# Optimization experiments

Hardware: AMD Instinct MI355X
Metric: run time of the kernel (lower is better)

## Reference

```python
import jax, jax.numpy as jnp
import numpy as np

IN_NC = 32
OUT_NC = 32
EXPAND = 2
HID = IN_NC * EXPAND          # 64
K = 3                         # depthwise kernel
EPS = 1e-5
R1 = IN_NC * HID              # end of pointwise-1 weights
R2 = R1 + HID * K * K         # end of depthwise weights
R3 = R2 + HID * OUT_NC        # total hyper params = 4672


def _bn(t, g, b):
    # BatchNorm2d in training mode over the flattened (b*fh*fw) batch:
    # stats over all axes except the channel axis (axis=3 of [b,fh,fw,C,H,W]).
    ax = (0, 1, 2, 4, 5)
    m = jnp.mean(t, axis=ax, keepdims=True)
    v = jnp.mean((t - m) ** 2, axis=ax, keepdims=True)
    sh = (1, 1, 1, -1, 1, 1)
    return (t - m) * jax.lax.rsqrt(v + EPS) * g.reshape(sh) + b.reshape(sh)


def _relu6(t):
    return jnp.clip(t, 0.0, 6.0)


def setup_inputs() -> dict:
    key = jax.random.key(0)
    k0, k1 = jax.random.split(key)
    x = jax.random.normal(k0, (8, IN_NC, 256, 256), dtype=jnp.float32)
    s = jax.random.normal(k1, (8, R3, 32, 32), dtype=jnp.float32) * 0.1
    return {
        'x': x,
        's': s,
        'gamma1': jnp.ones((HID,), jnp.float32),
        'beta1': jnp.zeros((HID,), jnp.float32),
        'gamma2': jnp.ones((HID,), jnp.float32),
        'beta2': jnp.zeros((HID,), jnp.float32),
        'gamma3': jnp.ones((OUT_NC,), jnp.float32),
        'beta3': jnp.zeros((OUT_NC,), jnp.float32),
    }


def reference(x, s, gamma1, beta1, gamma2, beta2, gamma3, beta3):
    b, c, h, w = x.shape
    fh, fw = s.shape[-2], s.shape[-1]
    ph, pw = h // fh, w // fw          # patch size
    kh, kw = ph + 2, pw + 2            # patch + reflect halo of 1

    # reflect-pad then extract overlapping [kh,kw] patches on a [ph,pw] grid
    xp = jnp.pad(x, ((0, 0), (0, 0), (1, 1), (1, 1)), mode='reflect')
    ri = (jnp.arange(fh) * ph)[:, None] + jnp.arange(kh)   # [fh,kh]
    ci = (jnp.arange(fw) * pw)[:, None] + jnp.arange(kw)   # [fw,kw]
    patches = xp[:, :, ri][:, :, :, :, ci]                 # [b,c,fh,kh,fw,kw]
    patches = patches.transpose(0, 2, 4, 1, 3, 5)          # [b,fh,fw,c,kh,kw]

    sw = s.transpose(0, 2, 3, 1)                           # [b,fh,fw,R3]

    # stage 1: per-patch 1x1 expand conv (in_nc -> hidden)
    w1 = sw[..., :R1].reshape(b, fh, fw, HID, c)
    y = jnp.einsum('bfgoc,bfgchw->bfgohw', w1, patches)    # [b,fh,fw,HID,kh,kw]
    y = _relu6(_bn(y, gamma1, beta1))

    # stage 2: per-patch depthwise 3x3 conv (valid), stride 1 -> [ph,pw]
    w2 = sw[..., R1:R2].reshape(b, fh, fw, HID, K, K)
    z = jnp.zeros((b, fh, fw, HID, ph, pw), y.dtype)
    for u in range(K):
        for v in range(K):
            z = z + w2[..., u, v, None, None] * y[..., u:u + ph, v:v + pw]
    z = _relu6(_bn(z, gamma2, beta2))

    # stage 3: per-patch 1x1 project conv (hidden -> out_nc)
    w3 = sw[..., R2:R3].reshape(b, fh, fw, OUT_NC, HID)
    o = jnp.einsum('bfgoc,bfgcpq->bfgopq', w3, z)          # [b,fh,fw,OUT_NC,ph,pw]
    o = _bn(o, gamma3, beta3)

    # reassemble patches: [b,fh,fw,C,ph,pw] -> [b,C,h,w]
    o = o.transpose(0, 3, 1, 4, 2, 5).reshape(b, OUT_NC, h, w)
    return x + o  # use_res_connect: stride==1 and in_nc==out_nc
```

## Files before the change

### kernel.cpp

```cpp
#include <hip/hip_runtime.h>

#define NT 256

constexpr int R1c = 2048;
constexpr int R2c = 2624;
constexpr float EPSc = 1e-5f;

constexpr int SLOTS1  = 0;
constexpr int SLOTS1Q = 4096;
constexpr int SLOTS2  = 8192;
constexpr int SLOTS2Q = 12288;
constexpr int SLOTS3  = 16384;
constexpr int SLOTS3Q = 18432;
constexpr int FIN1    = 20480;
constexpr int FIN2    = 20608;
constexpr int FIN3    = 20736;
constexpr int STATS_ZERO_FLOATS = 20480;

constexpr size_t ST2_OFF   = 131072;
constexpr size_t ST2_BYTES = 8ull * 1024 * 4672 * 2;
constexpr size_t ZB_OFF    = ST2_OFF + ST2_BYTES;
constexpr size_t ZB_BYTES  = 8192ull * 4096 * 2;
constexpr size_t OI_OFF    = ZB_OFF + ZB_BYTES;

__device__ __forceinline__ ushort f_to_bf16(float f) {
    union { float f; unsigned int i; } v; v.f = f;
    unsigned int r = (v.i + 0x7fffu + ((v.i >> 16) & 1u)) >> 16;
    return (ushort)r;
}
__device__ __forceinline__ float bf16_to_f(ushort u) {
    union { unsigned int i; float f; } v; v.i = ((unsigned int)u) << 16; return v.f;
}
__device__ __forceinline__ float bf16lo_to_f(unsigned int u) {
    union { unsigned int i; float f; } v; v.i = u << 16; return v.f;
}
__device__ __forceinline__ float bf16hi_to_f(unsigned int u) {
    union { unsigned int i; float f; } v; v.i = u & 0xffff0000u; return v.f;
}
__device__ __forceinline__ unsigned int pack_bf16(float lo, float hi) {
    return (unsigned int)f_to_bf16(lo) | ((unsigned int)f_to_bf16(hi) << 16);
}

typedef short bf16x8 __attribute__((ext_vector_type(8)));
typedef float f32x4  __attribute__((ext_vector_type(4)));
union FR { uint4 u4; bf16x8 v; ushort s[8]; };

__device__ __forceinline__ f32x4 mfma16(bf16x8 a, bf16x8 b, f32x4 c) {
    return __builtin_amdgcn_mfma_f32_16x16x32_bf16(a, b, c, 0, 0, 0);
}

__global__ __launch_bounds__(256)
void transpose_s_bf16p(const float* __restrict__ s, ushort* __restrict__ st) {
    __shared__ float tile[64][33];
    const int bi = blockIdx.z;
    const int p0 = blockIdx.x * 64;
    const int q0 = blockIdx.y * 32;
    const int tx = threadIdx.x, ty = threadIdx.y;
    const float* sb = s + (size_t)bi * 4672 * 1024;
    #pragma unroll
    for (int r = ty; r < 64; r += 8)
        tile[r][tx] = sb[(size_t)(p0 + r) * 1024 + q0 + tx];
    __syncthreads();
    unsigned int* stu = (unsigned int*)(st + (size_t)bi * 1024 * 4672);
    #pragma unroll
    for (int rr = ty; rr < 32; rr += 8) {
        int q = q0 + rr;
        unsigned int v = pack_bf16(tile[2*tx][rr], tile[2*tx + 1][rr]);
        stu[((size_t)q * 4672 + p0) / 2 + tx] = v;
    }
}


__global__ __launch_bounds__(NT, 4)
void k1_mf(const float* __restrict__ x, const ushort* __restrict__ st2,
           float* __restrict__ ws) {
    __shared__ ushort frB[4 * 3584];
    __shared__ float st1[128];
    const int t = threadIdx.x, blk = blockIdx.x;
    const int bi = blk >> 8, f = (blk >> 3) & 31, jb = blk & 7;
    const int g0 = jb * 4, slot = blk & 63;
    const int w = t >> 6, l = t & 63, l15 = l & 15, grp = l >> 4;

    if (t < 128) st1[t] = 0.f;
    {
        int p = t >> 6, e = t & 63;
        if ((e & 15) >= 4)
            ((uint4*)frB)[p * 448 + 384 + e] = make_uint4(0u, 0u, 0u, 0u);
    }
    const ushort* wp = st2 + (size_t)(bi * 1024 + f * 32 + g0 + w) * 4672;
    FR aw[4];
    #pragma unroll
    for (int m = 0; m < 4; m++) aw[m].u4 = ((const uint4*)wp)[(m * 16 + l15) * 4 + grp];

    const float* xb = x + (size_t)bi * 32 * 65536;
    for (int i = t; i < 3200; i += NT) {
        int c = i / 100, rem = i - c * 100;
        int r = rem / 10, seg = rem - r * 10;
        int row = f * 8 - 1 + r; row = row < 0 ? -row : (row > 255 ? 510 - row : row);
        int col0 = g0 * 8 - 4 + seg * 4;
        float v4[4];
        if (col0 >= 0 && col0 <= 252) {
            float4 vv = *(const float4*)(xb + (size_t)c * 65536 + row * 256 + col0);
            v4[0] = vv.x; v4[1] = vv.y; v4[2] = vv.z; v4[3] = vv.w;
        } else {
            #pragma unroll
            for (int d = 0; d < 4; d++) {
                int cc = col0 + d; cc = cc < 0 ? -cc : (cc > 255 ? 510 - cc : cc);
                v4[d] = xb[(size_t)c * 65536 + row * 256 + cc];
            }
        }
        int grpc = c >> 3, j = c & 7;
        #pragma unroll
        for (int d = 0; d < 4; d++) {
            int u = col0 + d - g0 * 8;
            ushort hv = f_to_bf16(v4[d]);
            #pragma unroll
            for (int p = 0; p < 4; p++) {
                int pc = u - 8 * p + 1;
                if (pc >= 0 && pc <= 9) {
                    int px = r * 10 + pc;
                    frB[p * 3584 + ((px >> 4) * 64 + grpc * 16 + (px & 15)) * 8 + j] = hv;
                }
            }
        }
    }
    __syncthreads();

    FR b[7];
    const uint4* bp = (const uint4*)(frB + w * 3584);
    #pragma unroll
    for (int n = 0; n < 7; n++) b[n].u4 = bp[n * 64 + l];
    float s4[16], q4[16];
    #pragma unroll
    for (int i = 0; i < 16; i++) { s4[i] = 0.f; q4[i] = 0.f; }
    #pragma unroll
    for (int m = 0; m < 4; m++) {
        #pragma unroll
        for (int n = 0; n < 7; n++) {
            f32x4 z = {0.f, 0.f, 0.f, 0.f};
            f32x4 c = mfma16(aw[m].v, b[n].v, z);
            #pragma unroll
            for (int r = 0; r < 4; r++) { float v = c[r]; s4[m*4+r] += v; q4[m*4+r] += v * v; }
        }
    }
    #pragma unroll
    for (int i = 0; i < 16; i++) {
        float sm = s4[i], qq = q4[i];
        #pragma unroll
        for (int msk = 1; msk <= 8; msk <<= 1) { sm += __shfl_xor(sm, msk); qq += __shfl_xor(qq, msk); }
        if (l15 == 0) {
            int ch = (i >> 2) * 16 + grp * 4 + (i & 3);
            atomicAdd(&st1[ch], sm);
            atomicAdd(&st1[64 + ch], qq);
        }
    }
    __syncthreads();
    if (t < 64) {
        atomicAdd(&ws[SLOTS1  + t * 64 + slot], st1[t]);
        atomicAdd(&ws[SLOTS1Q + t * 64 + slot], st1[64 + t]);
    }
}

__global__ __launch_bounds__(NT, 3)
void k2_mf(const float* __restrict__ x, const ushort* __restrict__ st2,
           ushort* __restrict__ zbuf, float* __restrict__ ws) {
    __shared__ ushort frB[4 * 3584];
    __shared__ unsigned int w2L[4 * 288];
    __shared__ float fin_s[128];
    const int t = threadIdx.x, blk = blockIdx.x;
    const int bi = blk >> 8, f = (blk >> 3) & 31, jb = blk & 7;
    const int g0 = jb * 4, slot = blk & 63;
    const int w = t >> 6, l = t & 63, l15 = l & 15, grp = l >> 4;
    const int patch = bi * 1024 + f * 32 + g0 + w;

    if (t < 128) fin_s[t] = ws[FIN1 + t];
    {
        int p = t >> 6, e = t & 63;
        if ((e & 15) >= 4)
            ((uint4*)frB)[p * 448 + 384 + e] = make_uint4(0u, 0u, 0u, 0u);
    }
    const ushort* wp = st2 + (size_t)patch * 4672;
    FR aw[4];
    #pragma unroll
    for (int m = 0; m < 4; m++) aw[m].u4 = ((const uint4*)wp)[(m * 16 + l15) * 4 + grp];
    for (int k = l; k < 288; k += 64) w2L[w * 288 + k] = ((const unsigned int*)(wp + R1c))[k];

    const float* xb = x + (size_t)bi * 32 * 65536;
    for (int i = t; i < 3200; i += NT) {
        int c = i / 100, rem = i - c * 100;
        int r = rem / 10, seg = rem - r * 10;
        int row = f * 8 - 1 + r; row = row < 0 ? -row : (row > 255 ? 510 - row : row);
        int col0 = g0 * 8 - 4 + seg * 4;
        float v4[4];
        if (col0 >= 0 && col0 <= 252) {
            float4 vv = *(const float4*)(xb + (size_t)c * 65536 + row * 256 + col0);
            v4[0] = vv.x; v4[1] = vv.y; v4[2] = vv.z; v4[3] = vv.w;
        } else {
            #pragma unroll
            for (int d = 0; d < 4; d++) {
                int cc = col0 + d; cc = cc < 0 ? -cc : (cc > 255 ? 510 - cc : cc);
                v4[d] = xb[(size_t)c * 65536 + row * 256 + cc];
            }
        }
        int grpc = c >> 3, j = c & 7;
        #pragma unroll
        for (int d = 0; d < 4; d++) {
            int u = col0 + d - g0 * 8;
            ushort hv = f_to_bf16(v4[d]);
            #pragma unroll
            for (int p = 0; p < 4; p++) {
                int pc = u - 8 * p + 1;
                if (pc >= 0 && pc <= 9) {
                    int px = r * 10 + pc;
                    frB[p * 3584 + ((px >> 4) * 64 + grpc * 16 + (px & 15)) * 8 + j] = hv;
                }
            }
        }
    }
    __syncthreads();

    FR b[7];
    const uint4* bp = (const uint4*)(frB + w * 3584);
    #pragma unroll
    for (int n = 0; n < 7; n++) b[n].u4 = bp[n * 64 + l];

    ushort* slice = frB + w * 3584;
    const ushort* w2u = (const ushort*)(w2L + w * 288);
    const int ch_l = l >> 2, quad = l & 3, p0 = quad * 2;
    float zsum[4], zsq[4];
    ushort* zp0 = zbuf + (size_t)patch * 4096;

    #pragma unroll
    for (int m = 0; m < 4; m++) {
        #pragma unroll
        for (int n = 0; n < 7; n++) {
            f32x4 z = {0.f, 0.f, 0.f, 0.f};
            f32x4 c = mfma16(aw[m].v, b[n].v, z);
            int px = n * 16 + l15;
            if (px < 100) {
                #pragma unroll
                for (int r = 0; r < 4; r++) {
                    int ch = m * 16 + grp * 4 + r;
                    float v = fminf(fmaxf(c[r] * fin_s[ch] + fin_s[64 + ch], 0.f), 6.f);
                    slice[(grp * 4 + r) * 102 + px] = f_to_bf16(v);
                }
            }
        }
        float yv[4][10];
        const unsigned int* sl32 = (const unsigned int*)slice;
        #pragma unroll
        for (int rr = 0; rr < 4; rr++) {
            int base = ch_l * 51 + (p0 + rr) * 5;
            #pragma unroll
            for (int k = 0; k < 5; k++) {
                unsigned int u = sl32[base + k];
                yv[rr][2*k] = bf16lo_to_f(u); yv[rr][2*k+1] = bf16hi_to_f(u);
            }
        }
        float wt[9];
        #pragma unroll
        for (int k = 0; k < 9; k++) wt[k] = bf16_to_f(w2u[(m * 16 + ch_l) * 9 + k]);
        float za[2][8];
        #pragma unroll
        for (int rr = 0; rr < 2; rr++)
            #pragma unroll
            for (int q = 0; q < 8; q++) za[rr][q] = 0.f;
        #pragma unroll
        for (int u = 0; u < 3; u++)
            #pragma unroll
            for (int v = 0; v < 3; v++) {
                float wv = wt[u * 3 + v];
                #pragma unroll
                for (int rr = 0; rr < 2; rr++)
                    #pragma unroll
                    for (int q = 0; q < 8; q++)
                        za[rr][q] += wv * yv[rr + u][q + v];
            }
        float zs = 0.f, zq = 0.f;
        #pragma unroll
        for (int rr = 0; rr < 2; rr++)
            #pragma unroll
            for (int q = 0; q < 8; q++) { float v = za[rr][q]; zs += v; zq += v * v; }
        zsum[m] = zs; zsq[m] = zq;
        ushort* zp = zp0 + (m * 16 + ch_l) * 64 + p0 * 8;
        uint4 pk0, pk1;
        pk0.x = pack_bf16(za[0][0], za[0][1]); pk0.y = pack_bf16(za[0][2], za[0][3]);
        pk0.z = pack_bf16(za[0][4], za[0][5]); pk0.w = pack_bf16(za[0][6], za[0][7]);
        pk1.x = pack_bf16(za[1][0], za[1][1]); pk1.y = pack_bf16(za[1][2], za[1][3]);
        pk1.z = pack_bf16(za[1][4], za[1][5]); pk1.w = pack_bf16(za[1][6], za[1][7]);
        *(uint4*)zp = pk0;
        *(uint4*)(zp + 8) = pk1;
    }
    __syncthreads();
    if (t < 128) fin_s[t] = 0.f;
    __syncthreads();
    #pragma unroll
    for (int m = 0; m < 4; m++) {
        float zs = zsum[m], zq = zsq[m];
        zs += __shfl_xor(zs, 1); zs += __shfl_xor(zs, 2);
        zq += __shfl_xor(zq, 1); zq += __shfl_xor(zq, 2);
        if (quad == 0) {
            atomicAdd(&fin_s[m * 16 + ch_l], zs);
            atomicAdd(&fin_s[64 + m * 16 + ch_l], zq);
        }
    }
    __syncthreads();
    if (t < 64) {
        atomicAdd(&ws[SLOTS2  + t * 64 + slot], fin_s[t]);
        atomicAdd(&ws[SLOTS2Q + t * 64 + slot], fin_s[64 + t]);
    }
}

__global__ __launch_bounds__(NT, 4)
void k3_mf(const ushort* __restrict__ zbuf, const ushort* __restrict__ st2,
           ushort* __restrict__ oi, float* __restrict__ ws) {
    __shared__ ushort zL[4 * 4224];
    __shared__ float fin2[128];
    __shared__ float st3[64];
    const int t = threadIdx.x, blk = blockIdx.x;
    const int bi = blk >> 8, f = (blk >> 3) & 31, jb = blk & 7;
    const int g0 = jb * 4, slot = blk & 63;
    const int w = t >> 6, l = t & 63, l15 = l & 15, grp = l >> 4;
    const int patch = bi * 1024 + f * 32 + g0 + w;

    if (t < 128) fin2[t] = ws[FIN2 + t];
    if (t >= 128 && t < 192) st3[t - 128] = 0.f;
    const ushort* wp = st2 + (size_t)patch * 4672;
    FR aw[2][2];
    #pragma unroll
    for (int m = 0; m < 2; m++)
        #pragma unroll
        for (int ks = 0; ks < 2; ks++)
            aw[m][ks].u4 = ((const uint4*)(wp + R2c))[(m * 16 + l15) * 8 + ks * 4 + grp];
    __syncthreads();

    const uint4* zsrc = (const uint4*)(zbuf + (size_t)patch * 4096);
    unsigned int* zd = (unsigned int*)zL;
    #pragma unroll
    for (int it = 0; it < 8; it++) {
        int i = l + 64 * it;
        uint4 v = zsrc[i];
        int ch = i >> 3, px0 = (i & 7) * 8;
        float a2 = fin2[ch], b2 = fin2[64 + ch];
        unsigned int uu[4] = {v.x, v.y, v.z, v.w};
        int base = w * 2112 + (ch * 66 + px0) / 2;
        #pragma unroll
        for (int k = 0; k < 4; k++) {
            float lo = fminf(fmaxf(bf16lo_to_f(uu[k]) * a2 + b2, 0.f), 6.f);
            float hi = fminf(fmaxf(bf16hi_to_f(uu[k]) * a2 + b2, 0.f), 6.f);
            zd[base + k] = pack_bf16(lo, hi);
        }
    }
    FR bfr[2][4];
    #pragma unroll
    for (int ks = 0; ks < 2; ks++)
        #pragma unroll
        for (int n = 0; n < 4; n++)
            #pragma unroll
            for (int j = 0; j < 8; j++)
                bfr[ks][n].s[j] = zL[w * 4224 + (ks * 32 + grp * 8 + j) * 66 + n * 16 + l15];

    float s4[2][4], q4[2][4];
    #pragma unroll
    for (int m = 0; m < 2; m++)
        #pragma unroll
        for (int r = 0; r < 4; r++) { s4[m][r] = 0.f; q4[m][r] = 0.f; }
    #pragma unroll
    for (int m = 0; m < 2; m++)
        #pragma unroll
        for (int n = 0; n < 4; n++) {
            f32x4 z = {0.f, 0.f, 0.f, 0.f};
            f32x4 c = mfma16(aw[m][0].v, bfr[0][n].v, z);
            c = mfma16(aw[m][1].v, bfr[1][n].v, c);
            #pragma unroll
            for (int r = 0; r < 4; r++) {
                float v = c[r];
                s4[m][r] += v; q4[m][r] += v * v;
                int oc = m * 16 + grp * 4 + r;
                int px = n * 16 + l15, p = px >> 3, q = px & 7;
                oi[((size_t)(bi * 32 + oc) * 256 + f * 8 + p) * 256 + (g0 + w) * 8 + q] = f_to_bf16(v);
            }
        }
    #pragma unroll
    for (int m = 0; m < 2; m++)
        #pragma unroll
        for (int r = 0; r < 4; r++) {
            float sm = s4[m][r], qq = q4[m][r];
            #pragma unroll
            for (int msk = 1; msk <= 8; msk <<= 1) { sm += __shfl_xor(sm, msk); qq += __shfl_xor(qq, msk); }
            if (l15 == 0) {
                int oc = m * 16 + grp * 4 + r;
                atomicAdd(&st3[oc], sm);
                atomicAdd(&st3[32 + oc], qq);
            }
        }
    __syncthreads();
    if (t < 32) {
        atomicAdd(&ws[SLOTS3  + t * 64 + slot], st3[t]);
        atomicAdd(&ws[SLOTS3Q + t * 64 + slot], st3[32 + t]);
    }
}

__global__ __launch_bounds__(NT, 8)
void k4_st(const float* __restrict__ x, const float* __restrict__ ws,
           const ushort* __restrict__ oi, float* __restrict__ out) {
    #pragma unroll
    for (int it = 0; it < 8; it++) {
        size_t e = ((size_t)(blockIdx.x * NT + threadIdx.x) + (size_t)it * (2048 * NT)) * 4;
        int oc = (int)((e >> 16) & 31);
        float a3 = ws[FIN3 + oc], b3 = ws[FIN3 + 32 + oc];
        uint2 ov = *(const uint2*)(oi + e);
        float4 xv = *(const float4*)(x + e);
        float4 r;
        r.x = xv.x + bf16lo_to_f(ov.x) * a3 + b3;
        r.y = xv.y + bf16hi_to_f(ov.x) * a3 + b3;
        r.z = xv.z + bf16lo_to_f(ov.y) * a3 + b3;
        r.w = xv.w + bf16hi_to_f(ov.y) * a3 + b3;
        *(float4*)(out + e) = r;
    }
}

__global__ void finalize_k(float* __restrict__ ws, int stage,
                           const float* __restrict__ gamma, const float* __restrict__ beta) {
    int ch = threadIdx.x;
    int nch = (stage == 3) ? 32 : 64;
    if (ch >= nch) return;
    int so = (stage == 1) ? SLOTS1  : (stage == 2) ? SLOTS2  : SLOTS3;
    int sq = (stage == 1) ? SLOTS1Q : (stage == 2) ? SLOTS2Q : SLOTS3Q;
    int fo = (stage == 1) ? FIN1    : (stage == 2) ? FIN2    : FIN3;
    float N = (stage == 1) ? 819200.0f : 524288.0f;
    float sm = 0.f, qq = 0.f;
    for (int j = 0; j < 64; j++) { sm += ws[so + ch*64 + j]; qq += ws[sq + ch*64 + j]; }
    float mean = sm / N;
    float var  = qq / N - mean * mean;
    float rstd = rsqrtf(var + EPSc);
    float a = rstd * gamma[ch];
    ws[fo + ch]       = a;
    ws[fo + nch + ch] = beta[ch] - mean * a;
}

extern "C" void kernel_launch(void* const* d_in, const int* in_sizes, int n_in,
                              void* d_out, int out_size, void* d_ws, size_t ws_size,
                              hipStream_t stream) {
    const float* x  = (const float*)d_in[0];
    const float* s  = (const float*)d_in[1];
    const float* g1 = (const float*)d_in[2];
    const float* b1 = (const float*)d_in[3];
    const float* g2 = (const float*)d_in[4];
    const float* b2 = (const float*)d_in[5];
    const float* g3 = (const float*)d_in[6];
    const float* b3 = (const float*)d_in[7];
    float* out = (float*)d_out;
    float* ws  = (float*)d_ws;

    hipMemsetAsync(d_ws, 0, STATS_ZERO_FLOATS * sizeof(float), stream);

    ushort* st2 = (ushort*)((char*)d_ws + ST2_OFF);
    ushort* zb  = (ushort*)((char*)d_ws + ZB_OFF);
    ushort* oi  = (ushort*)((char*)d_ws + OI_OFF);

    transpose_s_bf16p<<<dim3(73, 32, 8), dim3(32, 8), 0, stream>>>(s, st2);
    k1_mf<<<2048, NT, 0, stream>>>(x, st2, ws);
    finalize_k<<<1, 64, 0, stream>>>(ws, 1, g1, b1);
    k2_mf<<<2048, NT, 0, stream>>>(x, st2, zb, ws);
    finalize_k<<<1, 64, 0, stream>>>(ws, 2, g2, b2);
    k3_mf<<<2048, NT, 0, stream>>>(zb, st2, oi, ws);
    finalize_k<<<1, 64, 0, stream>>>(ws, 3, g3, b3);
    k4_st<<<2048, NT, 0, stream>>>(x, ws, oi, out);
}
```

Baseline: 298.8 us.

## Store stage-1 expand output in bf16 and skip recompute in stage 2

Stage 1 now writes its pointwise-expand result (pre-BN) as bf16 into a workspace buffer, staged through shared memory, and a new stage-2 kernel reads that buffer instead of reloading x and redoing the MFMA expand conv. This trades the recompute and the gather of x patches for roughly 109 MB of extra global writes and reads. The path is only taken when the workspace is large enough, with the old path kept as a fallback. The output buffer aliases the new y region, which is safe because y is consumed before stage 3 writes.

Result: faster. 284.8 us (-4.7%).

```diff
diff --git a/kernel.cpp b/kernel.cpp
--- a/kernel.cpp
+++ b/kernel.cpp
@@ -21,7 +21,10 @@
 constexpr size_t ST2_BYTES = 8ull * 1024 * 4672 * 2;
 constexpr size_t ZB_OFF    = ST2_OFF + ST2_BYTES;
 constexpr size_t ZB_BYTES  = 8192ull * 4096 * 2;
-constexpr size_t OI_OFF    = ZB_OFF + ZB_BYTES;
+constexpr size_t Y_OFF     = ZB_OFF + ZB_BYTES;
+constexpr size_t Y_BYTES   = 8192ull * 13312;
+constexpr size_t NEED_Y    = Y_OFF + Y_BYTES;
+constexpr size_t OI_OFF    = Y_OFF;
 
 __device__ __forceinline__ ushort f_to_bf16(float f) {
     union { float f; unsigned int i; } v; v.f = f;
@@ -70,16 +73,17 @@
     }
 }
 
-
+template<int SY>
 __global__ __launch_bounds__(NT, 4)
 void k1_mf(const float* __restrict__ x, const ushort* __restrict__ st2,
-           float* __restrict__ ws) {
+           ushort* __restrict__ ybuf, float* __restrict__ ws) {
     __shared__ ushort frB[4 * 3584];
     __shared__ float st1[128];
     const int t = threadIdx.x, blk = blockIdx.x;
     const int bi = blk >> 8, f = (blk >> 3) & 31, jb = blk & 7;
     const int g0 = jb * 4, slot = blk & 63;
     const int w = t >> 6, l = t & 63, l15 = l & 15, grp = l >> 4;
+    const int patch = bi * 1024 + f * 32 + g0 + w;
 
     if (t < 128) st1[t] = 0.f;
     {
@@ -87,7 +91,7 @@
         if ((e & 15) >= 4)
             ((uint4*)frB)[p * 448 + 384 + e] = make_uint4(0u, 0u, 0u, 0u);
     }
-    const ushort* wp = st2 + (size_t)(bi * 1024 + f * 32 + g0 + w) * 4672;
+    const ushort* wp = st2 + (size_t)patch * 4672;
     FR aw[4];
     #pragma unroll
     for (int m = 0; m < 4; m++) aw[m].u4 = ((const uint4*)wp)[(m * 16 + l15) * 4 + grp];
@@ -130,6 +134,11 @@
     const uint4* bp = (const uint4*)(frB + w * 3584);
     #pragma unroll
     for (int n = 0; n < 7; n++) b[n].u4 = bp[n * 64 + l];
+
+    ushort* slice = frB + w * 3584;
+    unsigned int* sliceU = (unsigned int*)slice;
+    uint4* yb4 = SY ? (((uint4*)ybuf) + (size_t)patch * 832) : nullptr;
+
     float s4[16], q4[16];
     #pragma unroll
     for (int i = 0; i < 16; i++) { s4[i] = 0.f; q4[i] = 0.f; }
@@ -139,8 +148,19 @@
         for (int n = 0; n < 7; n++) {
             f32x4 z = {0.f, 0.f, 0.f, 0.f};
             f32x4 c = mfma16(aw[m].v, b[n].v, z);
-            #pragma unroll
-            for (int r = 0; r < 4; r++) { float v = c[r]; s4[m*4+r] += v; q4[m*4+r] += v * v; }
+            int px = n * 16 + l15;
+            #pragma unroll
+            for (int r = 0; r < 4; r++) {
+                float v = c[r]; s4[m*4+r] += v; q4[m*4+r] += v * v;
+                if (SY && px < 100) slice[(grp * 4 + r) * 106 + px] = f_to_bf16(v);
+            }
+        }
+        if (SY) {
+            for (int i = l; i < 208; i += 64) {
+                int ch2 = i / 13, sub = i - ch2 * 13;
+                int ub = ch2 * 53 + sub * 4;
+                yb4[m * 208 + i] = make_uint4(sliceU[ub], sliceU[ub+1], sliceU[ub+2], sliceU[ub+3]);
+            }
         }
     }
     #pragma unroll
@@ -158,6 +178,111 @@
     if (t < 64) {
         atomicAdd(&ws[SLOTS1  + t * 64 + slot], st1[t]);
         atomicAdd(&ws[SLOTS1Q + t * 64 + slot], st1[64 + t]);
+    }
+}
+
+__global__ __launch_bounds__(NT, 4)
+void k2_y(const ushort* __restrict__ ybuf, const ushort* __restrict__ st2,
+          ushort* __restrict__ zbuf, float* __restrict__ ws) {
+    __shared__ ushort slc[4 * 1696];
+    __shared__ unsigned int w2L[4 * 288];
+    __shared__ float fin_s[128];
+    const int t = threadIdx.x, blk = blockIdx.x;
+    const int bi = blk >> 8, f = (blk >> 3) & 31, jb = blk & 7;
+    const int g0 = jb * 4, slot = blk & 63;
+    const int w = t >> 6, l = t & 63;
+    const int ch_l = l >> 2, quad = l & 3, p0 = quad * 2;
+    const int patch = bi * 1024 + f * 32 + g0 + w;
+
+    if (t < 128) fin_s[t] = ws[FIN1 + t];
+    const ushort* wp = st2 + (size_t)patch * 4672;
+    for (int k = l; k < 288; k += 64) w2L[w * 288 + k] = ((const unsigned int*)(wp + R1c))[k];
+    __syncthreads();
+
+    const uint4* yb4 = ((const uint4*)ybuf) + (size_t)patch * 832;
+    ushort* slice = slc + w * 1696;
+    unsigned int* sliceU = (unsigned int*)slice;
+    const ushort* w2u = (const ushort*)(w2L + w * 288);
+    ushort* zp0 = zbuf + (size_t)patch * 4096;
+    float zsum[4], zsq[4];
+
+    #pragma unroll
+    for (int m = 0; m < 4; m++) {
+        for (int i = l; i < 208; i += 64) {
+            uint4 v = yb4[m * 208 + i];
+            int ch2 = i / 13, sub = i - ch2 * 13;
+            int ch = m * 16 + ch2;
+            float a1 = fin_s[ch], b1 = fin_s[64 + ch];
+            unsigned int uu[4] = {v.x, v.y, v.z, v.w};
+            int ub = ch2 * 53 + sub * 4;
+            #pragma unroll
+            for (int k = 0; k < 4; k++) {
+                float lo = fminf(fmaxf(bf16lo_to_f(uu[k]) * a1 + b1, 0.f), 6.f);
+                float hi = fminf(fmaxf(bf16hi_to_f(uu[k]) * a1 + b1, 0.f), 6.f);
+                sliceU[ub + k] = pack_bf16(lo, hi);
+            }
+        }
+        float yv[4][10];
+        #pragma unroll
+        for (int rr = 0; rr < 4; rr++) {
+            int base = ch_l * 53 + (p0 + rr) * 5;
+            #pragma unroll
+            for (int k = 0; k < 5; k++) {
+                unsigned int u = sliceU[base + k];
+                yv[rr][2*k] = bf16lo_to_f(u); yv[rr][2*k+1] = bf16hi_to_f(u);
+            }
+        }
+        float wt[9];
+        #pragma unroll
+        for (int k = 0; k < 9; k++) wt[k] = bf16_to_f(w2u[(m * 16 + ch_l) * 9 + k]);
+        float za[2][8];
+        #pragma unroll
+        for (int rr = 0; rr < 2; rr++)
+            #pragma unroll
+            for (int q = 0; q < 8; q++) za[rr][q] = 0.f;
+        #pragma unroll
+        for (int u = 0; u < 3; u++)
+            #pragma unroll
+            for (int v = 0; v < 3; v++) {
+                float wv = wt[u * 3 + v];
+                #pragma unroll
+                for (int rr = 0; rr < 2; rr++)
+                    #pragma unroll
+                    for (int q = 0; q < 8; q++)
+                        za[rr][q] += wv * yv[rr + u][q + v];
+            }
+        float zs = 0.f, zq = 0.f;
+        #pragma unroll
+        for (int rr = 0; rr < 2; rr++)
+            #pragma unroll
+            for (int q = 0; q < 8; q++) { float v = za[rr][q]; zs += v; zq += v * v; }
+        zsum[m] = zs; zsq[m] = zq;
+        ushort* zp = zp0 + (m * 16 + ch_l) * 64 + p0 * 8;
+        uint4 pk0, pk1;
+        pk0.x = pack_bf16(za[0][0], za[0][1]); pk0.y = pack_bf16(za[0][2], za[0][3]);
+        pk0.z = pack_bf16(za[0][4], za[0][5]); pk0.w = pack_bf16(za[0][6], za[0][7]);
+        pk1.x = pack_bf16(za[1][0], za[1][1]); pk1.y = pack_bf16(za[1][2], za[1][3]);
+        pk1.z = pack_bf16(za[1][4], za[1][5]); pk1.w = pack_bf16(za[1][6], za[1][7]);
+        *(uint4*)zp = pk0;
+        *(uint4*)(zp + 8) = pk1;
+    }
+    __syncthreads();
+    if (t < 128) fin_s[t] = 0.f;
+    __syncthreads();
+    #pragma unroll
+    for (int m = 0; m < 4; m++) {
+        float zs = zsum[m], zq = zsq[m];
+        zs += __shfl_xor(zs, 1); zs += __shfl_xor(zs, 2);
+        zq += __shfl_xor(zq, 1); zq += __shfl_xor(zq, 2);
+        if (quad == 0) {
+            atomicAdd(&fin_s[m * 16 + ch_l], zs);
+            atomicAdd(&fin_s[64 + m * 16 + ch_l], zq);
+        }
+    }
+    __syncthreads();
+    if (t < 64) {
+        atomicAdd(&ws[SLOTS2  + t * 64 + slot], fin_s[t]);
+        atomicAdd(&ws[SLOTS2Q + t * 64 + slot], fin_s[64 + t]);
     }
 }
 
@@ -457,12 +582,21 @@
 
     ushort* st2 = (ushort*)((char*)d_ws + ST2_OFF);
     ushort* zb  = (ushort*)((char*)d_ws + ZB_OFF);
+    ushort* yb  = (ushort*)((char*)d_ws + Y_OFF);
     ushort* oi  = (ushort*)((char*)d_ws + OI_OFF);
 
+    const bool big = ws_size >= NEED_Y;
+
     transpose_s_bf16p<<<dim3(73, 32, 8), dim3(32, 8), 0, stream>>>(s, st2);
-    k1_mf<<<2048, NT, 0, stream>>>(x, st2, ws);
-    finalize_k<<<1, 64, 0, stream>>>(ws, 1, g1, b1);
-    k2_mf<<<2048, NT, 0, stream>>>(x, st2, zb, ws);
+    if (big) {
+        k1_mf<1><<<2048, NT, 0, stream>>>(x, st2, yb, ws);
+        finalize_k<<<1, 64, 0, stream>>>(ws, 1, g1, b1);
+        k2_y<<<2048, NT, 0, stream>>>(yb, st2, zb, ws);
+    } else {
+        k1_mf<0><<<2048, NT, 0, stream>>>(x, st2, nullptr, ws);
+        finalize_k<<<1, 64, 0, stream>>>(ws, 1, g1, b1);
+        k2_mf<<<2048, NT, 0, stream>>>(x, st2, zb, ws);
+    }
     finalize_k<<<1, 64, 0, stream>>>(ws, 2, g2, b2);
     k3_mf<<<2048, NT, 0, stream>>>(zb, st2, oi, ws);
     finalize_k<<<1, 64, 0, stream>>>(ws, 3, g3, b3);
```

## Fuse pipeline into cooperative persistent kernel and cache stage-1 output

Applied to the files above, without the earlier changes.

Replaces the multi-kernel launch sequence with one cooperative kernel that runs transpose, the three conv stages, the BN finalizes and the residual epilogue, separated by grid-wide syncs. This removes launch gaps, the memset and the finalize kernels. Stage 1 now writes the un-normalized expand-conv output to a new bf16 buffer, so stage 2 reads it instead of recomputing the patch gather and MFMA. Work units now cover two patches per block with waves split across channel halves. The trade-offs are grid.sync costs, an extra large intermediate buffer in HBM, and a fallback to separate kernels when the cooperative launch or workspace size fails.

Measured after the change: 790.7 us. +164.6%, slower.

```diff
diff --git a/kernel.cpp b/kernel.cpp
--- a/kernel.cpp
+++ b/kernel.cpp
@@ -1,4 +1,7 @@
 #include <hip/hip_runtime.h>
+#include <hip/hip_cooperative_groups.h>
+
+namespace cg = cooperative_groups;
 
 #define NT 256
 
@@ -21,7 +24,10 @@
 constexpr size_t ST2_BYTES = 8ull * 1024 * 4672 * 2;
 constexpr size_t ZB_OFF    = ST2_OFF + ST2_BYTES;
 constexpr size_t ZB_BYTES  = 8192ull * 4096 * 2;
-constexpr size_t OI_OFF    = ZB_OFF + ZB_BYTES;
+constexpr size_t Y_OFF     = ZB_OFF + ZB_BYTES;
+constexpr size_t Y_BYTES   = 8192ull * 13312;
+constexpr size_t NEED_Y    = Y_OFF + Y_BYTES;
+constexpr size_t OI_OFF    = Y_OFF;
 
 __device__ __forceinline__ ushort f_to_bf16(float f) {
     union { float f; unsigned int i; } v; v.f = f;
@@ -49,53 +55,55 @@
     return __builtin_amdgcn_mfma_f32_16x16x32_bf16(a, b, c, 0, 0, 0);
 }
 
-__global__ __launch_bounds__(256)
-void transpose_s_bf16p(const float* __restrict__ s, ushort* __restrict__ st) {
-    __shared__ float tile[64][33];
-    const int bi = blockIdx.z;
-    const int p0 = blockIdx.x * 64;
-    const int q0 = blockIdx.y * 32;
-    const int tx = threadIdx.x, ty = threadIdx.y;
+
+__device__ __forceinline__ void dev_transpose(int tile, int t,
+        const float* __restrict__ s, ushort* __restrict__ st, float* tl) {
+    const int bi = tile / (73 * 32);
+    int rem = tile - bi * 73 * 32;
+    const int qy = rem / 73, px = rem - qy * 73;
+    const int p0 = px * 64, q0 = qy * 32;
+    const int tx = t & 31, ty = t >> 5;
     const float* sb = s + (size_t)bi * 4672 * 1024;
     #pragma unroll
     for (int r = ty; r < 64; r += 8)
-        tile[r][tx] = sb[(size_t)(p0 + r) * 1024 + q0 + tx];
+        tl[r * 33 + tx] = sb[(size_t)(p0 + r) * 1024 + q0 + tx];
     __syncthreads();
     unsigned int* stu = (unsigned int*)(st + (size_t)bi * 1024 * 4672);
     #pragma unroll
     for (int rr = ty; rr < 32; rr += 8) {
         int q = q0 + rr;
-        unsigned int v = pack_bf16(tile[2*tx][rr], tile[2*tx + 1][rr]);
-        stu[((size_t)q * 4672 + p0) / 2 + tx] = v;
-    }
-}
-
-
-__global__ __launch_bounds__(NT, 4)
-void k1_mf(const float* __restrict__ x, const ushort* __restrict__ st2,
-           float* __restrict__ ws) {
-    __shared__ ushort frB[4 * 3584];
-    __shared__ float st1[128];
-    const int t = threadIdx.x, blk = blockIdx.x;
-    const int bi = blk >> 8, f = (blk >> 3) & 31, jb = blk & 7;
-    const int g0 = jb * 4, slot = blk & 63;
+        stu[((size_t)q * 4672 + p0) / 2 + tx] =
+            pack_bf16(tl[(2 * tx) * 33 + rr], tl[(2 * tx + 1) * 33 + rr]);
+    }
+    __syncthreads();
+}
+
+__device__ __forceinline__ void dev_k1(int unit, int t,
+        const float* __restrict__ x, const ushort* __restrict__ st2,
+        ushort* __restrict__ ybuf, float* __restrict__ ws,
+        ushort* frB, float* st1) {
+    const int bi = unit >> 9, f = (unit >> 4) & 31, jb = unit & 15;
+    const int g0 = jb * 2, slot = unit & 63;
     const int w = t >> 6, l = t & 63, l15 = l & 15, grp = l >> 4;
-
-    if (t < 128) st1[t] = 0.f;
-    {
+    const int pl_ = w >> 1, mh = w & 1;
+    const int patch = bi * 1024 + f * 32 + g0 + pl_;
+
+    if (t < 128) {
+        st1[t] = 0.f;
         int p = t >> 6, e = t & 63;
         if ((e & 15) >= 4)
             ((uint4*)frB)[p * 448 + 384 + e] = make_uint4(0u, 0u, 0u, 0u);
     }
-    const ushort* wp = st2 + (size_t)(bi * 1024 + f * 32 + g0 + w) * 4672;
-    FR aw[4];
-    #pragma unroll
-    for (int m = 0; m < 4; m++) aw[m].u4 = ((const uint4*)wp)[(m * 16 + l15) * 4 + grp];
+    const ushort* wp = st2 + (size_t)patch * 4672;
+    FR aw[2];
+    #pragma unroll
+    for (int i = 0; i < 2; i++)
+        aw[i].u4 = ((const uint4*)wp)[((mh * 2 + i) * 16 + l15) * 4 + grp];
 
     const float* xb = x + (size_t)bi * 32 * 65536;
-    for (int i = t; i < 3200; i += NT) {
-        int c = i / 100, rem = i - c * 100;
-        int r = rem / 10, seg = rem - r * 10;
+    for (int i = t; i < 1920; i += NT) {
+        int c = i / 60, rem = i - c * 60;
+        int r = rem / 6, seg = rem - r * 6;
         int row = f * 8 - 1 + r; row = row < 0 ? -row : (row > 255 ? 510 - row : row);
         int col0 = g0 * 8 - 4 + seg * 4;
         float v4[4];
@@ -115,7 +123,7 @@
             int u = col0 + d - g0 * 8;
             ushort hv = f_to_bf16(v4[d]);
             #pragma unroll
-            for (int p = 0; p < 4; p++) {
+            for (int p = 0; p < 2; p++) {
                 int pc = u - 8 * p + 1;
                 if (pc >= 0 && pc <= 9) {
                     int px = r * 10 + pc;
@@ -127,29 +135,44 @@
     __syncthreads();
 
     FR b[7];
-    const uint4* bp = (const uint4*)(frB + w * 3584);
+    const uint4* bp = (const uint4*)(frB + pl_ * 3584);
     #pragma unroll
     for (int n = 0; n < 7; n++) b[n].u4 = bp[n * 64 + l];
-    float s4[16], q4[16];
-    #pragma unroll
-    for (int i = 0; i < 16; i++) { s4[i] = 0.f; q4[i] = 0.f; }
-    #pragma unroll
-    for (int m = 0; m < 4; m++) {
+    __syncthreads();
+
+    ushort* slice = frB + pl_ * 3584 + mh * 1792;
+    unsigned int* sliceU = (unsigned int*)slice;
+    uint4* yb4 = (uint4*)ybuf + (size_t)patch * 832;
+    float s4[8], q4[8];
+    #pragma unroll
+    for (int i = 0; i < 8; i++) { s4[i] = 0.f; q4[i] = 0.f; }
+    #pragma unroll
+    for (int i = 0; i < 2; i++) {
+        int mm = mh * 2 + i;
         #pragma unroll
         for (int n = 0; n < 7; n++) {
             f32x4 z = {0.f, 0.f, 0.f, 0.f};
-            f32x4 c = mfma16(aw[m].v, b[n].v, z);
-            #pragma unroll
-            for (int r = 0; r < 4; r++) { float v = c[r]; s4[m*4+r] += v; q4[m*4+r] += v * v; }
-        }
-    }
-    #pragma unroll
-    for (int i = 0; i < 16; i++) {
+            f32x4 c = mfma16(aw[i].v, b[n].v, z);
+            int px = n * 16 + l15;
+            #pragma unroll
+            for (int r = 0; r < 4; r++) {
+                float v = c[r]; s4[i*4+r] += v; q4[i*4+r] += v * v;
+                if (px < 100) slice[(grp * 4 + r) * 106 + px] = f_to_bf16(v);
+            }
+        }
+        for (int k = l; k < 208; k += 64) {
+            int ch2 = k / 13, sub = k - ch2 * 13;
+            int ub = ch2 * 53 + sub * 4;
+            yb4[mm * 208 + k] = make_uint4(sliceU[ub], sliceU[ub+1], sliceU[ub+2], sliceU[ub+3]);
+        }
+    }
+    #pragma unroll
+    for (int i = 0; i < 8; i++) {
         float sm = s4[i], qq = q4[i];
         #pragma unroll
         for (int msk = 1; msk <= 8; msk <<= 1) { sm += __shfl_xor(sm, msk); qq += __shfl_xor(qq, msk); }
         if (l15 == 0) {
-            int ch = (i >> 2) * 16 + grp * 4 + (i & 3);
+            int ch = (mh * 2 + (i >> 2)) * 16 + grp * 4 + (i & 3);
             atomicAdd(&st1[ch], sm);
             atomicAdd(&st1[64 + ch], qq);
         }
@@ -159,107 +182,65 @@
         atomicAdd(&ws[SLOTS1  + t * 64 + slot], st1[t]);
         atomicAdd(&ws[SLOTS1Q + t * 64 + slot], st1[64 + t]);
     }
-}
-
-__global__ __launch_bounds__(NT, 3)
-void k2_mf(const float* __restrict__ x, const ushort* __restrict__ st2,
-           ushort* __restrict__ zbuf, float* __restrict__ ws) {
-    __shared__ ushort frB[4 * 3584];
-    __shared__ unsigned int w2L[4 * 288];
-    __shared__ float fin_s[128];
-    const int t = threadIdx.x, blk = blockIdx.x;
-    const int bi = blk >> 8, f = (blk >> 3) & 31, jb = blk & 7;
-    const int g0 = jb * 4, slot = blk & 63;
-    const int w = t >> 6, l = t & 63, l15 = l & 15, grp = l >> 4;
-    const int patch = bi * 1024 + f * 32 + g0 + w;
-
-    if (t < 128) fin_s[t] = ws[FIN1 + t];
-    {
-        int p = t >> 6, e = t & 63;
-        if ((e & 15) >= 4)
-            ((uint4*)frB)[p * 448 + 384 + e] = make_uint4(0u, 0u, 0u, 0u);
-    }
-    const ushort* wp = st2 + (size_t)patch * 4672;
-    FR aw[4];
-    #pragma unroll
-    for (int m = 0; m < 4; m++) aw[m].u4 = ((const uint4*)wp)[(m * 16 + l15) * 4 + grp];
-    for (int k = l; k < 288; k += 64) w2L[w * 288 + k] = ((const unsigned int*)(wp + R1c))[k];
-
-    const float* xb = x + (size_t)bi * 32 * 65536;
-    for (int i = t; i < 3200; i += NT) {
-        int c = i / 100, rem = i - c * 100;
-        int r = rem / 10, seg = rem - r * 10;
-        int row = f * 8 - 1 + r; row = row < 0 ? -row : (row > 255 ? 510 - row : row);
-        int col0 = g0 * 8 - 4 + seg * 4;
-        float v4[4];
-        if (col0 >= 0 && col0 <= 252) {
-            float4 vv = *(const float4*)(xb + (size_t)c * 65536 + row * 256 + col0);
-            v4[0] = vv.x; v4[1] = vv.y; v4[2] = vv.z; v4[3] = vv.w;
-        } else {
-            #pragma unroll
-            for (int d = 0; d < 4; d++) {
-                int cc = col0 + d; cc = cc < 0 ? -cc : (cc > 255 ? 510 - cc : cc);
-                v4[d] = xb[(size_t)c * 65536 + row * 256 + cc];
+    __syncthreads();
+}
+
+__device__ __forceinline__ void dev_k2(int unit, int t,
+        const ushort* __restrict__ ybuf, const ushort* __restrict__ st2,
+        ushort* __restrict__ zbuf, float* __restrict__ ws,
+        ushort* slc, unsigned int* w2L, const float* fin, float* acc) {
+    const int bi = unit >> 9, f = (unit >> 4) & 31, jb = unit & 15;
+    const int g0 = jb * 2, slot = unit & 63;
+    const int w = t >> 6, l = t & 63;
+    const int pl_ = w >> 1, mh = w & 1;
+    const int ch_l = l >> 2, quad = l & 3, p0 = quad * 2;
+    const int patch = bi * 1024 + f * 32 + g0 + pl_;
+
+    if (t < 128) acc[t] = 0.f;
+    for (int k = t; k < 576; k += NT) {
+        int p = (k >= 288) ? 1 : 0;
+        int kk = k - p * 288;
+        const unsigned int* src = (const unsigned int*)(st2 + (size_t)(bi*1024 + f*32 + g0 + p) * 4672 + R1c);
+        w2L[k] = src[kk];
+    }
+    __syncthreads();
+
+    const uint4* yb4 = (const uint4*)ybuf + (size_t)patch * 832;
+    ushort* slice = slc + w * 1696;
+    unsigned int* sliceU = (unsigned int*)slice;
+    const ushort* w2u = (const ushort*)(w2L + pl_ * 288);
+    ushort* zp0 = zbuf + (size_t)patch * 4096;
+
+    #pragma unroll
+    for (int i = 0; i < 2; i++) {
+        int mm = mh * 2 + i;
+        for (int k = l; k < 208; k += 64) {
+            uint4 v = yb4[mm * 208 + k];
+            int ch2 = k / 13, sub = k - ch2 * 13;
+            int ch = mm * 16 + ch2;
+            float a1 = fin[ch], b1 = fin[64 + ch];
+            unsigned int uu[4] = {v.x, v.y, v.z, v.w};
+            int ub = ch2 * 53 + sub * 4;
+            #pragma unroll
+            for (int kk = 0; kk < 4; kk++) {
+                float lo = fminf(fmaxf(bf16lo_to_f(uu[kk]) * a1 + b1, 0.f), 6.f);
+                float hi = fminf(fmaxf(bf16hi_to_f(uu[kk]) * a1 + b1, 0.f), 6.f);
+                sliceU[ub + kk] = pack_bf16(lo, hi);
             }
         }
-        int grpc = c >> 3, j = c & 7;
-        #pragma unroll
-        for (int d = 0; d < 4; d++) {
-            int u = col0 + d - g0 * 8;
-            ushort hv = f_to_bf16(v4[d]);
-            #pragma unroll
-            for (int p = 0; p < 4; p++) {
-                int pc = u - 8 * p + 1;
-                if (pc >= 0 && pc <= 9) {
-                    int px = r * 10 + pc;
-                    frB[p * 3584 + ((px >> 4) * 64 + grpc * 16 + (px & 15)) * 8 + j] = hv;
-                }
-            }
-        }
-    }
-    __syncthreads();
-
-    FR b[7];
-    const uint4* bp = (const uint4*)(frB + w * 3584);
-    #pragma unroll
-    for (int n = 0; n < 7; n++) b[n].u4 = bp[n * 64 + l];
-
-    ushort* slice = frB + w * 3584;
-    const ushort* w2u = (const ushort*)(w2L + w * 288);
-    const int ch_l = l >> 2, quad = l & 3, p0 = quad * 2;
-    float zsum[4], zsq[4];
-    ushort* zp0 = zbuf + (size_t)patch * 4096;
-
-    #pragma unroll
-    for (int m = 0; m < 4; m++) {
-        #pragma unroll
-        for (int n = 0; n < 7; n++) {
-            f32x4 z = {0.f, 0.f, 0.f, 0.f};
-            f32x4 c = mfma16(aw[m].v, b[n].v, z);
-            int px = n * 16 + l15;
-            if (px < 100) {
-                #pragma unroll
-                for (int r = 0; r < 4; r++) {
-                    int ch = m * 16 + grp * 4 + r;
-                    float v = fminf(fmaxf(c[r] * fin_s[ch] + fin_s[64 + ch], 0.f), 6.f);
-                    slice[(grp * 4 + r) * 102 + px] = f_to_bf16(v);
-                }
-            }
-        }
         float yv[4][10];
-        const unsigned int* sl32 = (const unsigned int*)slice;
         #pragma unroll
         for (int rr = 0; rr < 4; rr++) {
-            int base = ch_l * 51 + (p0 + rr) * 5;
+            int base = ch_l * 53 + (p0 + rr) * 5;
             #pragma unroll
             for (int k = 0; k < 5; k++) {
-                unsigned int u = sl32[base + k];
+                unsigned int u = sliceU[base + k];
                 yv[rr][2*k] = bf16lo_to_f(u); yv[rr][2*k+1] = bf16hi_to_f(u);
             }
         }
         float wt[9];
         #pragma unroll
-        for (int k = 0; k < 9; k++) wt[k] = bf16_to_f(w2u[(m * 16 + ch_l) * 9 + k]);
+        for (int k = 0; k < 9; k++) wt[k] = bf16_to_f(w2u[(mm * 16 + ch_l) * 9 + k]);
         float za[2][8];
         #pragma unroll
         for (int rr = 0; rr < 2; rr++)
@@ -281,8 +262,13 @@
         for (int rr = 0; rr < 2; rr++)
             #pragma unroll
             for (int q = 0; q < 8; q++) { float v = za[rr][q]; zs += v; zq += v * v; }
-        zsum[m] = zs; zsq[m] = zq;
-        ushort* zp = zp0 + (m * 16 + ch_l) * 64 + p0 * 8;
+        zs += __shfl_xor(zs, 1); zs += __shfl_xor(zs, 2);
+        zq += __shfl_xor(zq, 1); zq += __shfl_xor(zq, 2);
+        if (quad == 0) {
+            atomicAdd(&acc[mm * 16 + ch_l], zs);
+            atomicAdd(&acc[64 + mm * 16 + ch_l], zq);
+        }
+        ushort* zp = zp0 + (mm * 16 + ch_l) * 64 + p0 * 8;
         uint4 pk0, pk1;
         pk0.x = pack_bf16(za[0][0], za[0][1]); pk0.y = pack_bf16(za[0][2], za[0][3]);
         pk0.z = pack_bf16(za[0][4], za[0][5]); pk0.w = pack_bf16(za[0][6], za[0][7]);
@@ -292,58 +278,40 @@
         *(uint4*)(zp + 8) = pk1;
     }
     __syncthreads();
-    if (t < 128) fin_s[t] = 0.f;
-    __syncthreads();
-    #pragma unroll
-    for (int m = 0; m < 4; m++) {
-        float zs = zsum[m], zq = zsq[m];
-        zs += __shfl_xor(zs, 1); zs += __shfl_xor(zs, 2);
-        zq += __shfl_xor(zq, 1); zq += __shfl_xor(zq, 2);
-        if (quad == 0) {
-            atomicAdd(&fin_s[m * 16 + ch_l], zs);
-            atomicAdd(&fin_s[64 + m * 16 + ch_l], zq);
-        }
-    }
-    __syncthreads();
     if (t < 64) {
-        atomicAdd(&ws[SLOTS2  + t * 64 + slot], fin_s[t]);
-        atomicAdd(&ws[SLOTS2Q + t * 64 + slot], fin_s[64 + t]);
-    }
-}
-
-__global__ __launch_bounds__(NT, 4)
-void k3_mf(const ushort* __restrict__ zbuf, const ushort* __restrict__ st2,
-           ushort* __restrict__ oi, float* __restrict__ ws) {
-    __shared__ ushort zL[4 * 4224];
-    __shared__ float fin2[128];
-    __shared__ float st3[64];
-    const int t = threadIdx.x, blk = blockIdx.x;
-    const int bi = blk >> 8, f = (blk >> 3) & 31, jb = blk & 7;
-    const int g0 = jb * 4, slot = blk & 63;
+        atomicAdd(&ws[SLOTS2  + t * 64 + slot], acc[t]);
+        atomicAdd(&ws[SLOTS2Q + t * 64 + slot], acc[64 + t]);
+    }
+    __syncthreads();
+}
+
+__device__ __forceinline__ void dev_k3(int unit, int t,
+        const ushort* __restrict__ zbuf, const ushort* __restrict__ st2,
+        ushort* __restrict__ oi, float* __restrict__ ws,
+        ushort* zL, const float* fin, float* acc) {
+    const int bi = unit >> 9, f = (unit >> 4) & 31, jb = unit & 15;
+    const int g0 = jb * 2, slot = unit & 63;
     const int w = t >> 6, l = t & 63, l15 = l & 15, grp = l >> 4;
-    const int patch = bi * 1024 + f * 32 + g0 + w;
-
-    if (t < 128) fin2[t] = ws[FIN2 + t];
-    if (t >= 128 && t < 192) st3[t - 128] = 0.f;
+    const int pl_ = w >> 1, mh = w & 1;
+    const int patch = bi * 1024 + f * 32 + g0 + pl_;
+
+    if (t < 64) acc[t] = 0.f;
     const ushort* wp = st2 + (size_t)patch * 4672;
-    FR aw[2][2];
-    #pragma unroll
-    for (int m = 0; m < 2; m++)
-        #pragma unroll
-        for (int ks = 0; ks < 2; ks++)
-            aw[m][ks].u4 = ((const uint4*)(wp + R2c))[(m * 16 + l15) * 8 + ks * 4 + grp];
-    __syncthreads();
+    FR aw[2];
+    #pragma unroll
+    for (int ks = 0; ks < 2; ks++)
+        aw[ks].u4 = ((const uint4*)(wp + R2c))[(mh * 16 + l15) * 8 + ks * 4 + grp];
 
     const uint4* zsrc = (const uint4*)(zbuf + (size_t)patch * 4096);
     unsigned int* zd = (unsigned int*)zL;
     #pragma unroll
-    for (int it = 0; it < 8; it++) {
-        int i = l + 64 * it;
+    for (int it = 0; it < 4; it++) {
+        int i = mh * 256 + it * 64 + l;
         uint4 v = zsrc[i];
         int ch = i >> 3, px0 = (i & 7) * 8;
-        float a2 = fin2[ch], b2 = fin2[64 + ch];
+        float a2 = fin[ch], b2 = fin[64 + ch];
         unsigned int uu[4] = {v.x, v.y, v.z, v.w};
-        int base = w * 2112 + (ch * 66 + px0) / 2;
+        int base = pl_ * 2112 + (ch * 66 + px0) / 2;
         #pragma unroll
         for (int k = 0; k < 4; k++) {
             float lo = fminf(fmaxf(bf16lo_to_f(uu[k]) * a2 + b2, 0.f), 6.f);
@@ -351,6 +319,8 @@
             zd[base + k] = pack_bf16(lo, hi);
         }
     }
+    __syncthreads();
+
     FR bfr[2][4];
     #pragma unroll
     for (int ks = 0; ks < 2; ks++)
@@ -358,66 +328,163 @@
         for (int n = 0; n < 4; n++)
             #pragma unroll
             for (int j = 0; j < 8; j++)
-                bfr[ks][n].s[j] = zL[w * 4224 + (ks * 32 + grp * 8 + j) * 66 + n * 16 + l15];
-
-    float s4[2][4], q4[2][4];
-    #pragma unroll
-    for (int m = 0; m < 2; m++)
-        #pragma unroll
-        for (int r = 0; r < 4; r++) { s4[m][r] = 0.f; q4[m][r] = 0.f; }
-    #pragma unroll
-    for (int m = 0; m < 2; m++)
-        #pragma unroll
-        for (int n = 0; n < 4; n++) {
-            f32x4 z = {0.f, 0.f, 0.f, 0.f};
-            f32x4 c = mfma16(aw[m][0].v, bfr[0][n].v, z);
-            c = mfma16(aw[m][1].v, bfr[1][n].v, c);
-            #pragma unroll
-            for (int r = 0; r < 4; r++) {
-                float v = c[r];
-                s4[m][r] += v; q4[m][r] += v * v;
-                int oc = m * 16 + grp * 4 + r;
-                int px = n * 16 + l15, p = px >> 3, q = px & 7;
-                oi[((size_t)(bi * 32 + oc) * 256 + f * 8 + p) * 256 + (g0 + w) * 8 + q] = f_to_bf16(v);
-            }
-        }
-    #pragma unroll
-    for (int m = 0; m < 2; m++)
+                bfr[ks][n].s[j] = zL[pl_ * 4224 + (ks * 32 + grp * 8 + j) * 66 + n * 16 + l15];
+
+    float s4[4], q4[4];
+    #pragma unroll
+    for (int r = 0; r < 4; r++) { s4[r] = 0.f; q4[r] = 0.f; }
+    #pragma unroll
+    for (int n = 0; n < 4; n++) {
+        f32x4 z = {0.f, 0.f, 0.f, 0.f};
+        f32x4 c = mfma16(aw[0].v, bfr[0][n].v, z);
+        c = mfma16(aw[1].v, bfr[1][n].v, c);
         #pragma unroll
         for (int r = 0; r < 4; r++) {
-            float sm = s4[m][r], qq = q4[m][r];
-            #pragma unroll
-            for (int msk = 1; msk <= 8; msk <<= 1) { sm += __shfl_xor(sm, msk); qq += __shfl_xor(qq, msk); }
-            if (l15 == 0) {
-                int oc = m * 16 + grp * 4 + r;
-                atomicAdd(&st3[oc], sm);
-                atomicAdd(&st3[32 + oc], qq);
-            }
-        }
+            float v = c[r];
+            s4[r] += v; q4[r] += v * v;
+            int oc = mh * 16 + grp * 4 + r;
+            int px = n * 16 + l15, p = px >> 3, q = px & 7;
+            oi[((size_t)(bi * 32 + oc) * 256 + f * 8 + p) * 256 + (g0 + pl_) * 8 + q] = f_to_bf16(v);
+        }
+    }
+    #pragma unroll
+    for (int r = 0; r < 4; r++) {
+        float sm = s4[r], qq = q4[r];
+        #pragma unroll
+        for (int msk = 1; msk <= 8; msk <<= 1) { sm += __shfl_xor(sm, msk); qq += __shfl_xor(qq, msk); }
+        if (l15 == 0) {
+            int oc = mh * 16 + grp * 4 + r;
+            atomicAdd(&acc[oc], sm);
+            atomicAdd(&acc[32 + oc], qq);
+        }
+    }
     __syncthreads();
     if (t < 32) {
-        atomicAdd(&ws[SLOTS3  + t * 64 + slot], st3[t]);
-        atomicAdd(&ws[SLOTS3Q + t * 64 + slot], st3[32 + t]);
-    }
+        atomicAdd(&ws[SLOTS3  + t * 64 + slot], acc[t]);
+        atomicAdd(&ws[SLOTS3Q + t * 64 + slot], acc[32 + t]);
+    }
+    __syncthreads();
+}
+
+__device__ __forceinline__ void dev_k4(size_t base, int t,
+        const float* __restrict__ x, const ushort* __restrict__ oi,
+        float* __restrict__ out, const float* fin3) {
+    size_t e = (base + t) * 4;
+    int oc = (int)((e >> 16) & 31);
+    float a3 = fin3[oc], b3 = fin3[32 + oc];
+    uint2 ov = *(const uint2*)(oi + e);
+    float4 xv = *(const float4*)(x + e);
+    float4 r;
+    r.x = xv.x + bf16lo_to_f(ov.x) * a3 + b3;
+    r.y = xv.y + bf16hi_to_f(ov.x) * a3 + b3;
+    r.z = xv.z + bf16lo_to_f(ov.y) * a3 + b3;
+    r.w = xv.w + bf16hi_to_f(ov.y) * a3 + b3;
+    *(float4*)(out + e) = r;
+}
+
+__device__ __forceinline__ void dev_fin(const float* __restrict__ ws, int so, int sq,
+        const float* __restrict__ gamma, const float* __restrict__ beta,
+        int nch, float N, float* finL, int t) {
+    if (t < nch) {
+        float sm = 0.f, qq = 0.f;
+        for (int j = 0; j < 64; j++) { sm += ws[so + t*64 + j]; qq += ws[sq + t*64 + j]; }
+        float mean = sm / N;
+        float var  = qq / N - mean * mean;
+        float a = rsqrtf(var + EPSc) * gamma[t];
+        finL[t]       = a;
+        finL[nch + t] = beta[t] - mean * a;
+    }
+    __syncthreads();
+}
+
+__global__ __launch_bounds__(NT, 4)
+void fused_coop(const float* __restrict__ x, const float* __restrict__ s,
+                ushort* st2, ushort* ybuf, ushort* zbuf, ushort* oi,
+                float* ws,
+                const float* g1, const float* b1, const float* g2, const float* b2,
+                const float* g3, const float* b3, float* out) {
+    __shared__ __align__(16) char region[16896];
+    __shared__ float finL[128];
+    __shared__ float accL[128];
+    const int t = threadIdx.x, blk = blockIdx.x;
+    cg::grid_group grid = cg::this_grid();
+
+    {
+        int idx = blk * NT + t;
+        if (idx < STATS_ZERO_FLOATS) ws[idx] = 0.f;
+        float* tl = (float*)region;
+        for (int tile = blk; tile < 18688; tile += 1024)
+            dev_transpose(tile, t, s, st2, tl);
+    }
+    grid.sync();
+
+    for (int u = blk; u < 4096; u += 1024)
+        dev_k1(u, t, x, st2, ybuf, ws, (ushort*)region, accL);
+    grid.sync();
+
+    dev_fin(ws, SLOTS1, SLOTS1Q, g1, b1, 64, 819200.0f, finL, t);
+    for (int u = blk; u < 4096; u += 1024)
+        dev_k2(u, t, ybuf, st2, zbuf, ws, (ushort*)region,
+               (unsigned int*)(region + 13568), finL, accL);
+    grid.sync();
+
+    dev_fin(ws, SLOTS2, SLOTS2Q, g2, b2, 64, 524288.0f, finL, t);
+    for (int u = blk; u < 4096; u += 1024)
+        dev_k3(u, t, zbuf, st2, oi, ws, (ushort*)region, finL, accL);
+    grid.sync();
+
+    dev_fin(ws, SLOTS3, SLOTS3Q, g3, b3, 32, 524288.0f, finL, t);
+    #pragma unroll
+    for (int it = 0; it < 16; it++)
+        dev_k4((size_t)(it * 1024 + blk) * 256, t, x, oi, out, finL);
+}
+
+__global__ __launch_bounds__(256)
+void transpose_w(const float* __restrict__ s, ushort* __restrict__ st) {
+    __shared__ float tl[2112];
+    dev_transpose(blockIdx.x, threadIdx.x, s, st, tl);
+}
+
+__global__ __launch_bounds__(NT, 2)
+void k1_w(const float* __restrict__ x, const ushort* __restrict__ st2,
+          ushort* __restrict__ yb, float* __restrict__ ws) {
+    __shared__ __align__(16) ushort frB[2 * 3584];
+    __shared__ float st1[128];
+    dev_k1(blockIdx.x, threadIdx.x, x, st2, yb, ws, frB, st1);
+}
+
+__global__ __launch_bounds__(NT, 2)
+void k2_w(const ushort* __restrict__ yb, const ushort* __restrict__ st2,
+          ushort* __restrict__ zb, float* __restrict__ ws) {
+    __shared__ __align__(16) ushort slc[4 * 1696];
+    __shared__ unsigned int w2L[2 * 288];
+    __shared__ float finL[128];
+    __shared__ float accL[128];
+    if (threadIdx.x < 128) finL[threadIdx.x] = ws[FIN1 + threadIdx.x];
+    __syncthreads();
+    dev_k2(blockIdx.x, threadIdx.x, yb, st2, zb, ws, slc, w2L, finL, accL);
+}
+
+__global__ __launch_bounds__(NT, 2)
+void k3_w(const ushort* __restrict__ zb, const ushort* __restrict__ st2,
+          ushort* __restrict__ oi, float* __restrict__ ws) {
+    __shared__ __align__(16) ushort zL[2 * 4224];
+    __shared__ float finL[128];
+    __shared__ float accL[64];
+    if (threadIdx.x < 128) finL[threadIdx.x] = ws[FIN2 + threadIdx.x];
+    __syncthreads();
+    dev_k3(blockIdx.x, threadIdx.x, zb, st2, oi, ws, zL, finL, accL);
 }
 
 __global__ __launch_bounds__(NT, 8)
-void k4_st(const float* __restrict__ x, const float* __restrict__ ws,
-           const ushort* __restrict__ oi, float* __restrict__ out) {
-    #pragma unroll
-    for (int it = 0; it < 8; it++) {
-        size_t e = ((size_t)(blockIdx.x * NT + threadIdx.x) + (size_t)it * (2048 * NT)) * 4;
-        int oc = (int)((e >> 16) & 31);
-        float a3 = ws[FIN3 + oc], b3 = ws[FIN3 + 32 + oc];
-        uint2 ov = *(const uint2*)(oi + e);
-        float4 xv = *(const float4*)(x + e);
-        float4 r;
-        r.x = xv.x + bf16lo_to_f(ov.x) * a3 + b3;
-        r.y = xv.y + bf16hi_to_f(ov.x) * a3 + b3;
-        r.z = xv.z + bf16lo_to_f(ov.y) * a3 + b3;
-        r.w = xv.w + bf16hi_to_f(ov.y) * a3 + b3;
-        *(float4*)(out + e) = r;
-    }
+void k4_w(const float* __restrict__ x, const float* __restrict__ ws,
+          const ushort* __restrict__ oi, float* __restrict__ out) {
+    __shared__ float finL[64];
+    if (threadIdx.x < 64) finL[threadIdx.x] = ws[FIN3 + threadIdx.x];
+    __syncthreads();
+    #pragma unroll
+    for (int it = 0; it < 8; it++)
+        dev_k4((size_t)(it * 2048 + blockIdx.x) * 256, threadIdx.x, x, oi, out, finL);
 }
 
 __global__ void finalize_k(float* __restrict__ ws, int stage,
@@ -453,18 +520,30 @@
     float* out = (float*)d_out;
     float* ws  = (float*)d_ws;
 
-    hipMemsetAsync(d_ws, 0, STATS_ZERO_FLOATS * sizeof(float), stream);
-
     ushort* st2 = (ushort*)((char*)d_ws + ST2_OFF);
     ushort* zb  = (ushort*)((char*)d_ws + ZB_OFF);
+    ushort* yb  = (ushort*)((char*)d_ws + Y_OFF);
     ushort* oi  = (ushort*)((char*)d_ws + OI_OFF);
 
-    transpose_s_bf16p<<<dim3(73, 32, 8), dim3(32, 8), 0, stream>>>(s, st2);
-    k1_mf<<<2048, NT, 0, stream>>>(x, st2, ws);
+    if (ws_size >= NEED_Y) {
+        void* kargs[] = {
+            (void*)&x, (void*)&s, (void*)&st2, (void*)&yb, (void*)&zb, (void*)&oi,
+            (void*)&ws, (void*)&g1, (void*)&b1, (void*)&g2, (void*)&b2,
+            (void*)&g3, (void*)&b3, (void*)&out
+        };
+        hipError_t err = hipLaunchCooperativeKernel((void*)fused_coop,
+                                                    dim3(1024), dim3(NT),
+                                                    kargs, 0, stream);
+        if (err == hipSuccess) return;
+    }
+
+    hipMemsetAsync(d_ws, 0, STATS_ZERO_FLOATS * sizeof(float), stream);
+    transpose_w<<<18688, 256, 0, stream>>>(s, st2);
+    k1_w<<<4096, NT, 0, stream>>>(x, st2, yb, ws);
     finalize_k<<<1, 64, 0, stream>>>(ws, 1, g1, b1);
-    k2_mf<<<2048, NT, 0, stream>>>(x, st2, zb, ws);
+    k2_w<<<4096, NT, 0, stream>>>(yb, st2, zb, ws);
     finalize_k<<<1, 64, 0, stream>>>(ws, 2, g2, b2);
-    k3_mf<<<2048, NT, 0, stream>>>(zb, st2, oi, ws);
+    k3_w<<<4096, NT, 0, stream>>>(zb, st2, oi, ws);
     finalize_k<<<1, 64, 0, stream>>>(ws, 3, g3, b3);
-    k4_st<<<2048, NT, 0, stream>>>(x, ws, oi, out);
-}
+    k4_w<<<2048, NT, 0, stream>>>(x, ws, oi, out);
+}
```
